# Optimization experiments

Hardware: AMD Instinct MI355X
Metric: run time of the kernel (lower is better)

The kernel has to match this reference:

```python
import jax, jax.numpy as jnp
import numpy as np

HEADS = 8
GROUPS = 32
EPS = 1e-5


def setup_inputs() -> dict:
    key = jax.random.key(0)
    k_x, k_qkv, k_proj = jax.random.split(key, 3)
    B, C, H, W = 16, 512, 32, 32
    s = 0.02  # init scale for weights
    return {
        "x": jax.random.normal(k_x, (B, C, H, W), jnp.float32),
        "gn_scale": jnp.ones((C,), jnp.float32),
        "gn_bias": jnp.zeros((C,), jnp.float32),
        "w_qkv": jax.random.normal(k_qkv, (3 * C, C), jnp.float32) * s,
        "b_qkv": jnp.zeros((3 * C,), jnp.float32),
        "w_proj": jax.random.normal(k_proj, (C, C), jnp.float32) * s,
        "b_proj": jnp.zeros((C,), jnp.float32),
    }


def _group_norm(x, scale, bias):
    # x: [B, C, T]; GroupNorm32 computes stats in fp32
    B, C, T = x.shape
    xg = x.reshape(B, GROUPS, C // GROUPS, T).astype(jnp.float32)
    mu = xg.mean(axis=(2, 3), keepdims=True)
    var = xg.var(axis=(2, 3), keepdims=True)
    xn = ((xg - mu) * jax.lax.rsqrt(var + EPS)).reshape(B, C, T)
    return xn * scale[None, :, None] + bias[None, :, None]


def reference(x, gn_scale, gn_bias, w_qkv, b_qkv, w_proj, b_proj):
    B, C = x.shape[0], x.shape[1]
    T = int(np.prod(x.shape[2:]))
    xf = x.reshape(B, C, T)
    xn = _group_norm(xf, gn_scale, gn_bias).astype(x.dtype)
    # 1x1 conv == per-position matmul: [B, 3C, T]
    qkv = jnp.einsum('oc,bct->bot', w_qkv, xn) + b_qkv[None, :, None]
    ch = C // HEADS
    qkv = qkv.reshape(B * HEADS, 3 * ch, T)
    q, k, v = jnp.split(qkv, 3, axis=1)  # each [B*H, ch, T]
    scale = ch ** -0.25
    # scores: [B*H, T, T], softmax in fp32 (matches weight.float())
    w = jnp.einsum('bct,bcs->bts', q * scale, k * scale)
    w = jax.nn.softmax(w.astype(jnp.float32), axis=-1).astype(q.dtype)
    a = jnp.einsum('bts,bcs->bct', w, v).reshape(B, C, T)
    h = jnp.einsum('oc,bct->bot', w_proj, a) + b_proj[None, :, None]
    return (xf + h).reshape(x.shape)
```

## Files before the change

### kernel.cpp

```cpp
#include <hip/hip_runtime.h>
#include <cstdint>

#define NB 16
#define NC 512
#define NT 1024
#define NH 8
#define NG 32
#define GN_EPS 1e-5f
#define KSOFT 0.18033688011112042f

typedef float  f32x16 __attribute__((ext_vector_type(16)));
typedef __bf16 bf16x8 __attribute__((ext_vector_type(8)));
typedef unsigned int uint32x4 __attribute__((ext_vector_type(4)));

static __device__ __forceinline__ f32x16 zero16() {
    f32x16 z;
    #pragma unroll
    for (int i = 0; i < 16; ++i) z[i] = 0.f;
    return z;
}

static __device__ __forceinline__ f32x16 mfma(bf16x8 a, bf16x8 b, f32x16 c) {
    return __builtin_amdgcn_mfma_f32_32x32x16_bf16(a, b, c, 0, 0, 0);
}

static __device__ __forceinline__ unsigned pk2(float a, float b) {
    unsigned short x = __builtin_bit_cast(unsigned short, (__bf16)a);
    unsigned short y = __builtin_bit_cast(unsigned short, (__bf16)b);
    return (unsigned)x | ((unsigned)y << 16);
}

static __device__ __forceinline__ void swap32(unsigned& a, unsigned& b) {
#if __has_builtin(__builtin_amdgcn_permlane32_swap)
    auto r = __builtin_amdgcn_permlane32_swap(a, b, false, false);
    a = r[0];
    b = r[1];
#else
    unsigned sa = __shfl_xor(a, 32), sb = __shfl_xor(b, 32);
    bool hi = (threadIdx.x & 32) != 0;
    unsigned na = hi ? sb : a;
    unsigned nb = hi ? b : sa;
    a = na; b = nb;
#endif
}

static __device__ __forceinline__ bf16x8 lds_frag(const __bf16* base, int row, int sb) {
    const char* p = (const char*)base + row * 128 + (sb ^ ((row & 7) << 4));
    return *(const bf16x8*)p;
}

#define GLOAD16(gp, lp)                                                        \
    __builtin_amdgcn_global_load_lds(                                          \
        (const __attribute__((address_space(1))) unsigned int*)(gp),           \
        (__attribute__((address_space(3))) unsigned int*)(lp), 16, 0, 0)

__global__ __launch_bounds__(256) void fused_pre(
        const float* __restrict__ x, const float* __restrict__ gs,
        const float* __restrict__ gb, const float* __restrict__ w_qkv,
        const float* __restrict__ w_proj, __bf16* __restrict__ xnT,
        __bf16* __restrict__ wq_bf, __bf16* __restrict__ wp_bf)
{
    const int blk = blockIdx.x;
    const int thr = threadIdx.x;
    if (blk >= 128) {
        int i = (blk - 128) * 256 + thr;
        const float* src;
        __bf16* dst;
        if (i < 196608) { src = w_qkv; dst = wq_bf; }
        else            { i -= 196608; src = w_proj; dst = wp_bf; }
        float4 f = ((const float4*)src)[i];
        uint2 u;
        u.x = pk2(f.x, f.y);
        u.y = pk2(f.z, f.w);
        ((uint2*)dst)[i] = u;
        return;
    }
    const int b = blk >> 3, c0 = (blk & 7) * 64;
    __shared__ float gstat[8];
    {
        const int wv = thr >> 6, lane = thr & 63;
        const float* base = x + ((size_t)b * NC + c0 + wv * 16) * NT;
        float s = 0.f, s2 = 0.f;
        #pragma unroll
        for (int ch = 0; ch < 16; ++ch) {
            const float4* r4 = (const float4*)(base + (size_t)ch * NT);
            #pragma unroll
            for (int p = 0; p < 4; ++p) {
                float4 v = r4[lane + p * 64];
                s += v.x + v.y + v.z + v.w;
                s2 = fmaf(v.x, v.x, fmaf(v.y, v.y, fmaf(v.z, v.z, fmaf(v.w, v.w, s2))));
            }
        }
        #pragma unroll
        for (int off = 32; off; off >>= 1) {
            s  += __shfl_down(s, off);
            s2 += __shfl_down(s2, off);
        }
        if (lane == 0) {
            const float inv_n = 1.f / 16384.f;
            float mu  = s * inv_n;
            float var = s2 * inv_n - mu * mu;
            gstat[wv]     = mu;
            gstat[wv + 4] = rsqrtf(var + GN_EPS);
        }
    }
    __syncthreads();
    __shared__ float xs[64][65];
    const int tloc = thr & 63;
    for (int t0 = 0; t0 < NT; t0 += 64) {
        #pragma unroll
        for (int p = 0; p < 16; ++p) {
            int cr = p * 4 + (thr >> 6);
            int c = c0 + cr;
            float mu = gstat[cr >> 4];
            float rs = gstat[(cr >> 4) + 4];
            float v = x[((size_t)b * NC + c) * NT + t0 + tloc];
            xs[cr][tloc] = (v - mu) * rs * gs[c] + gb[c];
        }
        __syncthreads();
        const int cd = thr & 31;
        #pragma unroll
        for (int pp = 0; pp < 8; ++pp) {
            int tr = pp * 8 + (thr >> 5);
            unsigned w = pk2(xs[2 * cd][tr], xs[2 * cd + 1][tr]);
            size_t off = ((size_t)b * NT + t0 + tr) * NC + c0 + 2 * cd;
            *(unsigned*)((char*)xnT + off * 2) = w;
        }
        __syncthreads();
    }
}

__global__ __launch_bounds__(256) void qkv_gemm(const __bf16* __restrict__ wq,
                                                const __bf16* __restrict__ xnT,
                                                const float* __restrict__ bias,
                                                __bf16* __restrict__ qv,
                                                __bf16* __restrict__ kT)
{
    const int b = blockIdx.z, o0 = blockIdx.y * 128, t0 = blockIdx.x * 128;
    __shared__ __align__(16) char smem[32768];
    __bf16* wt = (__bf16*)smem;
    __bf16* xt = (__bf16*)(smem + 16384);
    const int thr = threadIdx.x;
    const int lane = thr & 63, wv = thr >> 6;
    const int lr = lane & 31, h = lane >> 5;
    const int wo = (wv >> 1) * 64, wn = (wv & 1) * 64;
    f32x16 acc[2][2];
    #pragma unroll
    for (int i = 0; i < 2; ++i)
        #pragma unroll
        for (int j = 0; j < 2; ++j) acc[i][j] = zero16();

    for (int kb = 0; kb < 8; ++kb) {
        const int c0 = kb * 64;
        __syncthreads();
        #pragma unroll
        for (int p = 0; p < 4; ++p) {
            int idx = p * 256 + thr, row = idx >> 3, sl = idx & 7;
            GLOAD16(wq + (size_t)(o0 + row) * NC + c0 + 8 * (sl ^ (row & 7)), wt + idx * 8);
            GLOAD16(xnT + ((size_t)b * NT + t0 + row) * NC + c0 + 8 * (sl ^ (row & 7)), xt + idx * 8);
        }
        asm volatile("s_waitcnt vmcnt(0)" ::: "memory");
        __syncthreads();
        #pragma unroll
        for (int kc = 0; kc < 4; ++kc) {
            bf16x8 a0 = lds_frag(wt, wo + lr,      32 * kc + 16 * h);
            bf16x8 a1 = lds_frag(wt, wo + 32 + lr, 32 * kc + 16 * h);
            bf16x8 b0 = lds_frag(xt, wn + lr,      32 * kc + 16 * h);
            bf16x8 b1 = lds_frag(xt, wn + 32 + lr, 32 * kc + 16 * h);
            acc[0][0] = mfma(a0, b0, acc[0][0]);
            acc[0][1] = mfma(a0, b1, acc[0][1]);
            acc[1][0] = mfma(a1, b0, acc[1][0]);
            acc[1][1] = mfma(a1, b1, acc[1][1]);
        }
    }

    char* ktile = smem;
    #pragma unroll
    for (int mt = 0; mt < 2; ++mt) {
        const int X = o0 + wo + 32 * mt;
        const int xm = X % 192;
        const int cat = xm >> 6;
        const int hd = X / 192;
        if (cat != 1) {
            #pragma unroll
            for (int nt = 0; nt < 2; ++nt)
                #pragma unroll
                for (int r = 0; r < 16; ++r) {
                    int off = (r & 3) + 8 * (r >> 2) + 4 * h;
                    int o = X + off;
                    int row = (cat == 0) ? (xm + off) : (xm - 64 + off);
                    int t = t0 + wn + 32 * nt + lr;
                    float v = acc[mt][nt][r] + bias[o];
                    if (cat == 0) v *= KSOFT;
                    qv[((size_t)(b * 8 + hd) * 128 + row) * NT + t] = (__bf16)v;
                }
        }
    }
    __syncthreads();
    #pragma unroll
    for (int mt = 0; mt < 2; ++mt) {
        const int X = o0 + wo + 32 * mt;
        const int xm = X % 192;
        if ((xm >> 6) == 1) {
            #pragma unroll
            for (int nt = 0; nt < 2; ++nt) {
                int t_local = wn + 32 * nt + lr;
                #pragma unroll
                for (int g = 0; g < 4; ++g) {
                    int ob = X + 8 * g + 4 * h;
                    int cb = (xm - 64) + 8 * g + 4 * h;
                    uint2 d;
                    d.x = pk2(acc[mt][nt][4 * g + 0] + bias[ob + 0],
                              acc[mt][nt][4 * g + 1] + bias[ob + 1]);
                    d.y = pk2(acc[mt][nt][4 * g + 2] + bias[ob + 2],
                              acc[mt][nt][4 * g + 3] + bias[ob + 3]);
                    *(uint2*)(ktile + t_local * 144 + cb * 2) = d;
                }
            }
        }
    }
    if ((o0 % 192) != 128) {
        __syncthreads();
        const int khd = o0 / 192;
        #pragma unroll
        for (int pass = 0; pass < 4; ++pass) {
            int t_local = pass * 32 + (thr >> 3);
            int c8 = thr & 7;
            uint32x4 d = *(const uint32x4*)(ktile + t_local * 144 + c8 * 16);
            *(uint32x4*)(kT + ((size_t)(b * 8 + khd) * 1024 + t0 + t_local) * 64 + c8 * 8) = d;
        }
    }
}

#define PP(R) ((R) < 16 ? p0[(R) & 15] : p1[(R) & 15])

__global__ __launch_bounds__(256, 4) void attn_mfma(const __bf16* __restrict__ qv,
                                                    const __bf16* __restrict__ kT,
                                                    __bf16* __restrict__ aT)
{
    const int wg = blockIdx.x;
    const int orig = (wg & 7) * 128 + (wg >> 3);
    const int tq0 = (orig & 7) * 128;
    const int bh = orig >> 3;
    const int b = bh >> 3, hd = bh & 7;
    const __bf16* qg = qv + (size_t)bh * 128 * NT;
    const __bf16* vg = qg + (size_t)64 * NT;
    const __bf16* kTg = kT + (size_t)bh * 1024 * 64;
    const int thr = threadIdx.x, lane = thr & 63, wv = thr >> 6;
    const int lr = lane & 31, h = lane >> 5;
    const int tw = tq0 + wv * 32;
    __shared__ __align__(16) char smem[32768];
    __bf16* kb0 = (__bf16*)smem;
    __bf16* vb0 = (__bf16*)(smem + 8192);
    __bf16* kb1 = (__bf16*)(smem + 16384);
    __bf16* vb1 = (__bf16*)(smem + 24576);

    bf16x8 qf[4];
    {
        const unsigned short* qs = (const unsigned short*)qg;
        #pragma unroll
        for (int kc = 0; kc < 4; ++kc) {
            unsigned w[4];
            #pragma unroll
            for (int ww = 0; ww < 4; ++ww) {
                int c0 = 16 * kc + 8 * h + 2 * ww;
                unsigned lo = qs[(size_t)c0 * NT + tw + lr];
                unsigned hi = qs[(size_t)(c0 + 1) * NT + tw + lr];
                w[ww] = lo | (hi << 16);
            }
            uint32x4 u = {w[0], w[1], w[2], w[3]};
            qf[kc] = __builtin_bit_cast(bf16x8, u);
        }
    }
    bf16x8 ones;
    #pragma unroll
    for (int i = 0; i < 8; ++i) ones[i] = (__bf16)1.0f;

    f32x16 oacc0 = zero16(), oacc1 = zero16(), sacc = zero16();

    const __bf16* kbase[2];
    const __bf16* vbase[2];
    int ldsoff[2];
    #pragma unroll
    for (int p = 0; p < 2; ++p) {
        int idx = p * 256 + thr, row = idx >> 3, sl = idx & 7;
        kbase[p] = kTg + (size_t)row * 64 + 8 * (sl ^ (row & 7));
        vbase[p] = vg + (size_t)row * NT + 8 * (sl ^ (row & 7));
        ldsoff[p] = idx * 8;
    }

    #pragma unroll
    for (int p = 0; p < 2; ++p) {
        GLOAD16(kbase[p], kb0 + ldsoff[p]);
        GLOAD16(vbase[p], vb0 + ldsoff[p]);
    }

    for (int it = 0; it < 16; ++it) {
        __bf16* kcur = (it & 1) ? kb1 : kb0;
        __bf16* vcur = (it & 1) ? vb1 : vb0;
        if (it < 15) {
            __bf16* knxt = (it & 1) ? kb0 : kb1;
            __bf16* vnxt = (it & 1) ? vb0 : vb1;
            const int s0 = (it + 1) * 64;
            #pragma unroll
            for (int p = 0; p < 2; ++p) {
                GLOAD16(kbase[p] + (size_t)s0 * 64, knxt + ldsoff[p]);
                GLOAD16(vbase[p] + s0, vnxt + ldsoff[p]);
            }
            asm volatile("s_waitcnt vmcnt(4)" ::: "memory");
        } else {
            asm volatile("s_waitcnt vmcnt(0)" ::: "memory");
        }
        __builtin_amdgcn_s_barrier();

        f32x16 p0 = zero16(), p1 = zero16();
        __builtin_amdgcn_s_setprio(1);
        #pragma unroll
        for (int kc = 0; kc < 4; ++kc) {
            bf16x8 ka0 = lds_frag(kcur, lr,      32 * kc + 16 * h);
            bf16x8 ka1 = lds_frag(kcur, 32 + lr, 32 * kc + 16 * h);
            p0 = mfma(ka0, qf[kc], p0);
            p1 = mfma(ka1, qf[kc], p1);
        }
        __builtin_amdgcn_s_setprio(0);

        #pragma unroll
        for (int r = 0; r < 16; ++r) {
            p0[r] = exp2f(p0[r]);
            p1[r] = exp2f(p1[r]);
        }

        #pragma unroll
        for (int ks = 0; ks < 4; ++ks) {
            const int Rb = 16 * (ks >> 1) + 8 * (ks & 1);
            unsigned a0 = pk2(PP(Rb + 0), PP(Rb + 1));
            unsigned c0 = pk2(PP(Rb + 2), PP(Rb + 3));
            unsigned a1 = pk2(PP(Rb + 4), PP(Rb + 5));
            unsigned c1 = pk2(PP(Rb + 6), PP(Rb + 7));
            swap32(a0, a1);
            swap32(c0, c1);
            uint32x4 u = {a0, c0, a1, c1};
            bf16x8 pf = __builtin_bit_cast(bf16x8, u);
            bf16x8 v0 = lds_frag(vcur, lr,      32 * ks + 16 * h);
            bf16x8 v1 = lds_frag(vcur, 32 + lr, 32 * ks + 16 * h);
            __builtin_amdgcn_s_setprio(1);
            oacc0 = mfma(v0, pf, oacc0);
            oacc1 = mfma(v1, pf, oacc1);
            sacc  = mfma(ones, pf, sacc);
            __builtin_amdgcn_s_setprio(0);
        }
        __builtin_amdgcn_s_barrier();
    }

    float inv = 1.f / sacc[0];
    char* at = smem;
    {
        int t_local = wv * 32 + lr;
        #pragma unroll
        for (int g = 0; g < 4; ++g) {
            int cb = 8 * g + 4 * h;
            uint2 d0, d1;
            d0.x = pk2(oacc0[4 * g + 0] * inv, oacc0[4 * g + 1] * inv);
            d0.y = pk2(oacc0[4 * g + 2] * inv, oacc0[4 * g + 3] * inv);
            *(uint2*)(at + t_local * 144 + cb * 2) = d0;
            d1.x = pk2(oacc1[4 * g + 0] * inv, oacc1[4 * g + 1] * inv);
            d1.y = pk2(oacc1[4 * g + 2] * inv, oacc1[4 * g + 3] * inv);
            *(uint2*)(at + t_local * 144 + (cb + 32) * 2) = d1;
        }
    }
    __syncthreads();
    #pragma unroll
    for (int pass = 0; pass < 4; ++pass) {
        int t_local = pass * 32 + (thr >> 3);
        int c8 = thr & 7;
        uint32x4 d = *(const uint32x4*)(at + t_local * 144 + c8 * 16);
        *(uint32x4*)(aT + ((size_t)b * NT + tq0 + t_local) * NC + hd * 64 + c8 * 8) = d;
    }
}

__global__ __launch_bounds__(256) void proj_gemm(const __bf16* __restrict__ wp,
                                                 const __bf16* __restrict__ aT,
                                                 const float* __restrict__ bias,
                                                 const float* __restrict__ x,
                                                 float* __restrict__ out)
{
    const int b = blockIdx.z, o0 = blockIdx.y * 128, t0 = blockIdx.x * 128;
    __shared__ __align__(16) char smem[32768];
    __bf16* wt = (__bf16*)smem;
    __bf16* xt = (__bf16*)(smem + 16384);
    const int thr = threadIdx.x;
    const int lane = thr & 63, wv = thr >> 6;
    const int lr = lane & 31, h = lane >> 5;
    const int wo = (wv >> 1) * 64, wn = (wv & 1) * 64;
    f32x16 acc[2][2];
    #pragma unroll
    for (int i = 0; i < 2; ++i)
        #pragma unroll
        for (int j = 0; j < 2; ++j) acc[i][j] = zero16();

    for (int kb = 0; kb < 8; ++kb) {
        const int c0 = kb * 64;
        __syncthreads();
        #pragma unroll
        for (int p = 0; p < 4; ++p) {
            int idx = p * 256 + thr, row = idx >> 3, sl = idx & 7;
            GLOAD16(wp + (size_t)(o0 + row) * NC + c0 + 8 * (sl ^ (row & 7)), wt + idx * 8);
            GLOAD16(aT + ((size_t)b * NT + t0 + row) * NC + c0 + 8 * (sl ^ (row & 7)), xt + idx * 8);
        }
        asm volatile("s_waitcnt vmcnt(0)" ::: "memory");
        __syncthreads();
        #pragma unroll
        for (int kc = 0; kc < 4; ++kc) {
            bf16x8 a0 = lds_frag(wt, wo + lr,      32 * kc + 16 * h);
            bf16x8 a1 = lds_frag(wt, wo + 32 + lr, 32 * kc + 16 * h);
            bf16x8 b0 = lds_frag(xt, wn + lr,      32 * kc + 16 * h);
            bf16x8 b1 = lds_frag(xt, wn + 32 + lr, 32 * kc + 16 * h);
            acc[0][0] = mfma(a0, b0, acc[0][0]);
            acc[0][1] = mfma(a0, b1, acc[0][1]);
            acc[1][0] = mfma(a1, b0, acc[1][0]);
            acc[1][1] = mfma(a1, b1, acc[1][1]);
        }
    }
    #pragma unroll
    for (int mt = 0; mt < 2; ++mt)
        #pragma unroll
        for (int nt = 0; nt < 2; ++nt)
            #pragma unroll
            for (int r = 0; r < 16; ++r) {
                int o = o0 + wo + 32 * mt + (r & 3) + 8 * (r >> 2) + 4 * h;
                int t = t0 + wn + 32 * nt + lr;
                size_t off = ((size_t)b * NC + o) * NT + t;
                out[off] = acc[mt][nt][r] + bias[o] + x[off];
            }
}

extern "C" void kernel_launch(void* const* d_in, const int* in_sizes, int n_in,
                              void* d_out, int out_size, void* d_ws, size_t ws_size,
                              hipStream_t stream)
{
    const float* x       = (const float*)d_in[0];
    const float* gnscale = (const float*)d_in[1];
    const float* gnbias  = (const float*)d_in[2];
    const float* w_qkv   = (const float*)d_in[3];
    const float* b_qkv   = (const float*)d_in[4];
    const float* w_proj  = (const float*)d_in[5];
    const float* b_proj  = (const float*)d_in[6];
    float* out = (float*)d_out;

    char* ws = (char*)d_ws;
    __bf16* wq_bf = (__bf16*)(ws + 4096);
    __bf16* wp_bf = (__bf16*)(ws + 1576960);
    __bf16* xnT   = (__bf16*)(ws + 2101248);
    __bf16* qv    = (__bf16*)(ws + 18878464);
    __bf16* kTb   = (__bf16*)(ws + 52432896);
    __bf16* aTb   = (__bf16*)(ws + 69210112);

    fused_pre<<<1152, 256, 0, stream>>>(x, gnscale, gnbias, w_qkv, w_proj,
                                        xnT, wq_bf, wp_bf);
    qkv_gemm<<<dim3(8, 12, NB), 256, 0, stream>>>(wq_bf, xnT, b_qkv, qv, kTb);
    attn_mfma<<<1024, 256, 0, stream>>>(qv, kTb, aTb);
    proj_gemm<<<dim3(8, 4, NB), 256, 0, stream>>>(wp_bf, aTb, b_proj, x, out);
}
```

Measured before the change: 151.2 us.

## Load K/V MFMA fragments directly from global memory instead of LDS staging

Drops the double-buffered LDS staging of K and V tiles, along with its async global-to-LDS loads, waitcnts and barriers. Each wave now reads its K and V fragments straight from global memory into registers, relying on L2/cache for reuse across the four waves of a workgroup. The shared buffer shrinks to hold only the output epilogue, which may raise occupancy. In exchange, each wave issues its own redundant global loads, with no explicit prefetch to hide their latency.

```diff
diff --git a/kernel.cpp b/kernel.cpp
--- a/kernel.cpp
+++ b/kernel.cpp
@@ -249,11 +249,7 @@
     const int thr = threadIdx.x, lane = thr & 63, wv = thr >> 6;
     const int lr = lane & 31, h = lane >> 5;
     const int tw = tq0 + wv * 32;
-    __shared__ __align__(16) char smem[32768];
-    __bf16* kb0 = (__bf16*)smem;
-    __bf16* vb0 = (__bf16*)(smem + 8192);
-    __bf16* kb1 = (__bf16*)(smem + 16384);
-    __bf16* vb1 = (__bf16*)(smem + 24576);
+    __shared__ __align__(16) char smem[18432];
 
     bf16x8 qf[4];
     {
@@ -278,49 +274,26 @@
 
     f32x16 oacc0 = zero16(), oacc1 = zero16(), sacc = zero16();
 
-    const __bf16* kbase[2];
-    const __bf16* vbase[2];
-    int ldsoff[2];
-    #pragma unroll
-    for (int p = 0; p < 2; ++p) {
-        int idx = p * 256 + thr, row = idx >> 3, sl = idx & 7;
-        kbase[p] = kTg + (size_t)row * 64 + 8 * (sl ^ (row & 7));
-        vbase[p] = vg + (size_t)row * NT + 8 * (sl ^ (row & 7));
-        ldsoff[p] = idx * 8;
-    }
-
-    #pragma unroll
-    for (int p = 0; p < 2; ++p) {
-        GLOAD16(kbase[p], kb0 + ldsoff[p]);
-        GLOAD16(vbase[p], vb0 + ldsoff[p]);
-    }
-
+    const __bf16* kfb0 = kTg + (size_t)lr * 64 + 8 * h;
+    const __bf16* kfb1 = kTg + (size_t)(32 + lr) * 64 + 8 * h;
+    const __bf16* vfb0 = vg + (size_t)lr * NT + 8 * h;
+    const __bf16* vfb1 = vg + (size_t)(32 + lr) * NT + 8 * h;
+
+    #pragma unroll 2
     for (int it = 0; it < 16; ++it) {
-        __bf16* kcur = (it & 1) ? kb1 : kb0;
-        __bf16* vcur = (it & 1) ? vb1 : vb0;
-        if (it < 15) {
-            __bf16* knxt = (it & 1) ? kb0 : kb1;
-            __bf16* vnxt = (it & 1) ? vb0 : vb1;
-            const int s0 = (it + 1) * 64;
-            #pragma unroll
-            for (int p = 0; p < 2; ++p) {
-                GLOAD16(kbase[p] + (size_t)s0 * 64, knxt + ldsoff[p]);
-                GLOAD16(vbase[p] + s0, vnxt + ldsoff[p]);
-            }
-            asm volatile("s_waitcnt vmcnt(4)" ::: "memory");
-        } else {
-            asm volatile("s_waitcnt vmcnt(0)" ::: "memory");
-        }
-        __builtin_amdgcn_s_barrier();
-
+        const int s0 = it * 64;
+        bf16x8 ka0[4], ka1[4];
+        #pragma unroll
+        for (int kc = 0; kc < 4; ++kc) {
+            ka0[kc] = *(const bf16x8*)(kfb0 + (size_t)s0 * 64 + 16 * kc);
+            ka1[kc] = *(const bf16x8*)(kfb1 + (size_t)s0 * 64 + 16 * kc);
+        }
         f32x16 p0 = zero16(), p1 = zero16();
         __builtin_amdgcn_s_setprio(1);
         #pragma unroll
         for (int kc = 0; kc < 4; ++kc) {
-            bf16x8 ka0 = lds_frag(kcur, lr,      32 * kc + 16 * h);
-            bf16x8 ka1 = lds_frag(kcur, 32 + lr, 32 * kc + 16 * h);
-            p0 = mfma(ka0, qf[kc], p0);
-            p1 = mfma(ka1, qf[kc], p1);
+            p0 = mfma(ka0[kc], qf[kc], p0);
+            p1 = mfma(ka1[kc], qf[kc], p1);
         }
         __builtin_amdgcn_s_setprio(0);
 
@@ -341,15 +314,14 @@
             swap32(c0, c1);
             uint32x4 u = {a0, c0, a1, c1};
             bf16x8 pf = __builtin_bit_cast(bf16x8, u);
-            bf16x8 v0 = lds_frag(vcur, lr,      32 * ks + 16 * h);
-            bf16x8 v1 = lds_frag(vcur, 32 + lr, 32 * ks + 16 * h);
+            bf16x8 v0 = *(const bf16x8*)(vfb0 + s0 + 16 * ks);
+            bf16x8 v1 = *(const bf16x8*)(vfb1 + s0 + 16 * ks);
             __builtin_amdgcn_s_setprio(1);
             oacc0 = mfma(v0, pf, oacc0);
             oacc1 = mfma(v1, pf, oacc1);
             sacc  = mfma(ones, pf, sacc);
             __builtin_amdgcn_s_setprio(0);
         }
-        __builtin_amdgcn_s_barrier();
     }
 
     float inv = 1.f / sacc[0];
```

Result: slower. 226.4 us (+49.8%).
